# Kernel optimization log

Measured on AMD Instinct MI355X. Metric: run time of the kernel, lower is better.

Reference implementation:

```python
import jax, jax.numpy as jnp
import numpy as np

B, T, C = 2, 1024, 768
H, NE, K = 3072, 8, 2


def setup_inputs() -> dict:
    key = jax.random.key(0)
    k1, k2, k3, k4 = jax.random.split(key, 4)
    x = jax.random.normal(k1, (B, T, C), dtype=jnp.float32)
    w_fc = jax.random.normal(k2, (C, H * NE), dtype=jnp.float32) * 0.02
    w_proj = jax.random.normal(k3, (H * NE, C), dtype=jnp.float32) * (0.02 * (2 * 12) ** -0.5)
    w_gate = jax.random.normal(k4, (C, NE), dtype=jnp.float32) * 0.02
    return {"x": x, "w_fc": w_fc, "w_proj": w_proj, "w_gate": w_gate}


def reference(x, w_fc, w_proj, w_gate):
    # Router: softmax over experts, top-k, renormalize selected probs.
    router_logits = jnp.einsum('btc,ce->bte', x, w_gate)
    router_probs = jax.nn.softmax(router_logits, axis=-1)
    top_p, top_i = jax.lax.top_k(router_probs, K)          # (B,T,K)
    top_p = top_p / jnp.sum(top_p, axis=-1, keepdims=True)

    # First projection. Original gathers (C,H,B,T,K) weight slices then
    # einsum('btc,chbtk->bthk'); mathematically identical to projecting with
    # all experts and gathering the selected outputs (same contraction order).
    wf = w_fc.reshape(C, H, NE)
    h_all = jnp.einsum('btc,che->bthe', x, wf)             # (B,T,H,NE)
    h = jnp.take_along_axis(h_all, top_i[:, :, None, :], axis=-1)  # (B,T,H,K)
    h = jax.nn.gelu(h, approximate=True)

    # Second projection + weighted combine over the K selected experts.
    wp = w_proj.reshape(H, C, NE)
    o_all = jnp.einsum('bthk,hce->btcke', h, wp)           # (B,T,C,K,NE)
    o = jnp.take_along_axis(o_all, top_i[:, :, None, :, None], axis=-1)[..., 0]  # (B,T,C,K)
    o = jnp.einsum('btck,btk->btc', o, top_p)
    return o
```

## Files before the change

kernel.cpp:

```cpp
#include <hip/hip_runtime.h>
#include <hip/hip_bf16.h>
#include <math.h>

#define BB 2
#define TT 1024
#define CC 768
#define HH 3072
#define NEXP 8
#define NTOK (BB*TT)
#define CAP 1024
#define CNT_STRIDE 32

typedef __attribute__((ext_vector_type(8))) short short8;
typedef __attribute__((ext_vector_type(4))) float float4v;

typedef const __attribute__((address_space(1))) void* gptr_t;
typedef __attribute__((address_space(3))) void* sptr_t;

__device__ __forceinline__ unsigned short f2bf(float f) {
    unsigned int u = __float_as_uint(f);
    unsigned int r = (u + 0x7fffu + ((u >> 16) & 1u)) >> 16;
    return (unsigned short)r;
}
__device__ __forceinline__ float gelu_tanh(float v) {
    const float k2 = 2.0f * 0.7978845608028654f;
    const float k1 = 0.044715f;
    float z = k2 * (v + k1 * v * v * v);
    return v / (1.0f + __expf(-z));
}

__device__ __forceinline__ void permute_body(
        const float* __restrict__ In, unsigned short* __restrict__ Out,
        int Adim, int Bdim, int a0, int b0, unsigned short* L) {
    int t = threadIdx.x;
#pragma unroll
    for (int j = 0; j < 8; ++j) {
        int idx = j * 256 + t;
        int r = idx >> 4, c4 = idx & 15;
        const float4 v = *(const float4*)(In + (size_t)(a0 + r) * Bdim * 8 + b0 * 8 + c4 * 4);
        ushort2 s01, s23;
        s01.x = f2bf(v.x); s01.y = f2bf(v.y);
        s23.x = f2bf(v.z); s23.y = f2bf(v.w);
        *(ushort2*)&L[r * 66 + c4 * 4]     = s01;
        *(ushort2*)&L[r * 66 + c4 * 4 + 2] = s23;
    }
    __syncthreads();
    int w = t >> 6, ln = t & 63;
    int oc = w * 16 + (ln & 15);
    int e = oc & 7, b = b0 + (oc >> 3);
    unsigned short* dst = Out + ((size_t)e * Bdim + b) * Adim + a0;
#pragma unroll
    for (int p = 0; p < 4; ++p) {
        int seg = (ln >> 4) + p * 4;
        short8 vv;
#pragma unroll
        for (int k = 0; k < 8; ++k) vv[k] = (short)L[(seg * 8 + k) * 66 + oc];
        *(short8*)(dst + seg * 8) = vv;
    }
}

__device__ __forceinline__ void router_body(
        const float* __restrict__ x, const float* __restrict__ w_gate,
        float* __restrict__ top_p, int* __restrict__ counts,
        int* __restrict__ tok_list, int t) {
    int lane = threadIdx.x & 63;
    float acc[NEXP];
#pragma unroll
    for (int e = 0; e < NEXP; ++e) acc[e] = 0.f;
    for (int c = lane; c < CC; c += 64) {
        float xv = x[t * CC + c];
        const float4* wg = (const float4*)(w_gate + c * NEXP);
        float4 w0 = wg[0], w1 = wg[1];
        acc[0] += xv * w0.x; acc[1] += xv * w0.y;
        acc[2] += xv * w0.z; acc[3] += xv * w0.w;
        acc[4] += xv * w1.x; acc[5] += xv * w1.y;
        acc[6] += xv * w1.z; acc[7] += xv * w1.w;
    }
#pragma unroll
    for (int e = 0; e < NEXP; ++e) {
        for (int off = 32; off > 0; off >>= 1)
            acc[e] += __shfl_down(acc[e], off, 64);
    }
    if (lane == 0) {
        float m = acc[0];
#pragma unroll
        for (int e = 1; e < NEXP; ++e) m = fmaxf(m, acc[e]);
        float p[NEXP]; float s = 0.f;
#pragma unroll
        for (int e = 0; e < NEXP; ++e) { p[e] = expf(acc[e] - m); s += p[e]; }
        float inv_s = 1.f / s;
#pragma unroll
        for (int e = 0; e < NEXP; ++e) p[e] *= inv_s;
        int i0 = 0;
#pragma unroll
        for (int e = 1; e < NEXP; ++e) if (p[e] > p[i0]) i0 = e;
        int i1 = (i0 == 0) ? 1 : 0;
#pragma unroll
        for (int e = 0; e < NEXP; ++e) if (e != i0 && p[e] > p[i1]) i1 = e;
        float p0 = p[i0], p1 = p[i1];
        float inv = 1.f / (p0 + p1);
        top_p[t * 2 + 0] = p0 * inv;
        top_p[t * 2 + 1] = p1 * inv;
        int pos0 = atomicAdd(&counts[i0 * CNT_STRIDE], 1);
        if (pos0 < CAP) tok_list[i0 * NTOK + pos0] = t * 2 + 0;
        int pos1 = atomicAdd(&counts[i1 * CNT_STRIDE], 1);
        if (pos1 < CAP) tok_list[i1 * NTOK + pos1] = t * 2 + 1;
    }
}

__global__ __launch_bounds__(256)
void mega_pre(const float* __restrict__ w_fc, unsigned short* __restrict__ wfc_b,
              const float* __restrict__ w_proj, unsigned short* __restrict__ wp_b,
              const float* __restrict__ x, const float* __restrict__ w_gate,
              float* __restrict__ top_p, int* __restrict__ counts,
              int* __restrict__ tok_list) {
    __shared__ unsigned short L[128 * 66];
    int bid = blockIdx.x;
    if (bid < 2304) {
        permute_body(w_fc, wfc_b, CC, HH, (bid % 6) * 128, (bid / 6) * 8, L);
    } else if (bid < 4608) {
        int b2 = bid - 2304;
        permute_body(w_proj, wp_b, HH, CC, (b2 % 24) * 128, (b2 / 24) * 8, L);
    } else {
        int wave = threadIdx.x >> 6;
        int t = (bid - 4608) * 4 + wave;
        router_body(x, w_gate, top_p, counts, tok_list, t);
    }
}

__global__ void gather_x(const float* __restrict__ x,
                         const int* __restrict__ counts,
                         const int* __restrict__ tok_list,
                         unsigned short* __restrict__ xg) {
    int pos = blockIdx.x;
    int e = pos >> 10, i = pos & (CAP - 1);
    int M = counts[e * CNT_STRIDE]; if (M > CAP) M = CAP;
    int Mr = (M + 127) & ~127; if (Mr > CAP) Mr = CAP;
    if (i >= Mr) return;
    int c = threadIdx.x * 4;
    unsigned short* dst = xg + (size_t)pos * CC + c;
    ushort4 s;
    if (i < M) {
        int tk = tok_list[e * NTOK + i] >> 1;
        float4 v = *(const float4*)(x + (size_t)tk * CC + c);
        s.x = f2bf(v.x); s.y = f2bf(v.y); s.z = f2bf(v.z); s.w = f2bf(v.w);
    } else {
        s.x = s.y = s.z = s.w = 0;
    }
    *(ushort4*)dst = s;
}

__global__ __launch_bounds__(256)
void gemm1_mfma(const unsigned short* __restrict__ xg,
                const unsigned short* __restrict__ wfc_b,
                const int* __restrict__ counts,
                unsigned short* __restrict__ h_slab) {
    int e = blockIdx.z;
    int M = counts[e * CNT_STRIDE]; if (M > CAP) M = CAP;
    int m0 = blockIdx.y * 128;
    if (m0 >= M) return;
    int n0 = blockIdx.x * 128;

    __shared__ unsigned short As[2][128 * 32];
    __shared__ unsigned short Bs[2][128 * 32];

    int tid = threadIdx.x;
    int wave = tid >> 6, lane = tid & 63;
    int wm = wave >> 1, wn = wave & 1;
    int quad = lane >> 4, l16 = lane & 15;

    const unsigned short* aBase = xg + ((size_t)e * CAP + m0) * CC;
    const unsigned short* bBase = wfc_b + ((size_t)e * HH + n0) * CC;

    int srow = wave * 32 + (lane >> 2);
    int schunk = (lane & 3) * 8;

    float4v acc[4][4];
#pragma unroll
    for (int i = 0; i < 4; ++i)
#pragma unroll
        for (int j = 0; j < 4; ++j)
#pragma unroll
            for (int r = 0; r < 4; ++r) acc[i][j][r] = 0.f;

#pragma unroll
    for (int q = 0; q < 2; ++q) {
        int r = srow + q * 16;
        __builtin_amdgcn_global_load_lds(
            (gptr_t)(aBase + (size_t)r * CC + schunk),
            (sptr_t)(&As[0][(wave * 32 + q * 16) * 32]), 16, 0, 0);
        __builtin_amdgcn_global_load_lds(
            (gptr_t)(bBase + (size_t)r * CC + schunk),
            (sptr_t)(&Bs[0][(wave * 32 + q * 16) * 32]), 16, 0, 0);
    }

    for (int k0 = 0; k0 < CC; k0 += 32) {
        int cur = (k0 >> 5) & 1;
        __syncthreads();
        if (k0 + 32 < CC) {
            int nxt = cur ^ 1;
#pragma unroll
            for (int q = 0; q < 2; ++q) {
                int r = srow + q * 16;
                __builtin_amdgcn_global_load_lds(
                    (gptr_t)(aBase + (size_t)r * CC + k0 + 32 + schunk),
                    (sptr_t)(&As[nxt][(wave * 32 + q * 16) * 32]), 16, 0, 0);
                __builtin_amdgcn_global_load_lds(
                    (gptr_t)(bBase + (size_t)r * CC + k0 + 32 + schunk),
                    (sptr_t)(&Bs[nxt][(wave * 32 + q * 16) * 32]), 16, 0, 0);
            }
        }
        short8 af[4], bf[4];
#pragma unroll
        for (int mt = 0; mt < 4; ++mt)
            af[mt] = *(const short8*)&As[cur][(wm * 64 + mt * 16 + l16) * 32 + quad * 8];
#pragma unroll
        for (int nt = 0; nt < 4; ++nt)
            bf[nt] = *(const short8*)&Bs[cur][(wn * 64 + nt * 16 + l16) * 32 + quad * 8];
#pragma unroll
        for (int mt = 0; mt < 4; ++mt)
#pragma unroll
            for (int nt = 0; nt < 4; ++nt)
                acc[mt][nt] = __builtin_amdgcn_mfma_f32_16x16x32_bf16(
                    af[mt], bf[nt], acc[mt][nt], 0, 0, 0);
    }

#pragma unroll
    for (int mt = 0; mt < 4; ++mt) {
#pragma unroll
        for (int r = 0; r < 4; ++r) {
            int m = m0 + wm * 64 + mt * 16 + quad * 4 + r;
            unsigned short* orow = h_slab + ((size_t)e * CAP + m) * HH + n0 + wn * 64 + l16;
#pragma unroll
            for (int nt = 0; nt < 4; ++nt)
                orow[nt * 16] = f2bf(gelu_tanh(acc[mt][nt][r]));
        }
    }
}

__global__ __launch_bounds__(256)
void gemm2_mfma(const unsigned short* __restrict__ h_slab,
                const unsigned short* __restrict__ wp_b,
                const int* __restrict__ counts,
                const int* __restrict__ tok_list,
                float* __restrict__ o_part) {
    int e = blockIdx.z;
    int M = counts[e * CNT_STRIDE]; if (M > CAP) M = CAP;
    int m0 = blockIdx.y * 128;
    if (m0 >= M) return;
    int n0 = (blockIdx.x >> 2) * 128;
    int ks = blockIdx.x & 3;

    __shared__ unsigned short As[2][128 * 32];
    __shared__ unsigned short Bs[2][128 * 32];

    int tid = threadIdx.x;
    int wave = tid >> 6, lane = tid & 63;
    int wm = wave >> 1, wn = wave & 1;
    int quad = lane >> 4, l16 = lane & 15;

    const unsigned short* aBase = h_slab + ((size_t)e * CAP + m0) * HH + ks * 768;
    const unsigned short* bBase = wp_b + ((size_t)e * CC + n0) * HH + ks * 768;

    int srow = wave * 32 + (lane >> 2);
    int schunk = (lane & 3) * 8;

    float4v acc[4][4];
#pragma unroll
    for (int i = 0; i < 4; ++i)
#pragma unroll
        for (int j = 0; j < 4; ++j)
#pragma unroll
            for (int r = 0; r < 4; ++r) acc[i][j][r] = 0.f;

#pragma unroll
    for (int q = 0; q < 2; ++q) {
        int r = srow + q * 16;
        __builtin_amdgcn_global_load_lds(
            (gptr_t)(aBase + (size_t)r * HH + schunk),
            (sptr_t)(&As[0][(wave * 32 + q * 16) * 32]), 16, 0, 0);
        __builtin_amdgcn_global_load_lds(
            (gptr_t)(bBase + (size_t)r * HH + schunk),
            (sptr_t)(&Bs[0][(wave * 32 + q * 16) * 32]), 16, 0, 0);
    }

    for (int k0 = 0; k0 < 768; k0 += 32) {
        int cur = (k0 >> 5) & 1;
        __syncthreads();
        if (k0 + 32 < 768) {
            int nxt = cur ^ 1;
#pragma unroll
            for (int q = 0; q < 2; ++q) {
                int r = srow + q * 16;
                __builtin_amdgcn_global_load_lds(
                    (gptr_t)(aBase + (size_t)r * HH + k0 + 32 + schunk),
                    (sptr_t)(&As[nxt][(wave * 32 + q * 16) * 32]), 16, 0, 0);
                __builtin_amdgcn_global_load_lds(
                    (gptr_t)(bBase + (size_t)r * HH + k0 + 32 + schunk),
                    (sptr_t)(&Bs[nxt][(wave * 32 + q * 16) * 32]), 16, 0, 0);
            }
        }
        short8 af[4], bf[4];
#pragma unroll
        for (int mt = 0; mt < 4; ++mt)
            af[mt] = *(const short8*)&As[cur][(wm * 64 + mt * 16 + l16) * 32 + quad * 8];
#pragma unroll
        for (int nt = 0; nt < 4; ++nt)
            bf[nt] = *(const short8*)&Bs[cur][(wn * 64 + nt * 16 + l16) * 32 + quad * 8];
#pragma unroll
        for (int mt = 0; mt < 4; ++mt)
#pragma unroll
            for (int nt = 0; nt < 4; ++nt)
                acc[mt][nt] = __builtin_amdgcn_mfma_f32_16x16x32_bf16(
                    af[mt], bf[nt], acc[mt][nt], 0, 0, 0);
    }

#pragma unroll
    for (int mt = 0; mt < 4; ++mt) {
#pragma unroll
        for (int r = 0; r < 4; ++r) {
            int m = m0 + wm * 64 + mt * 16 + quad * 4 + r;
            if (m < M) {
                int ent = tok_list[e * NTOK + m];
                float* orow = o_part + ((size_t)ks * NTOK * 2 + ent) * CC + n0 + wn * 64 + l16;
#pragma unroll
                for (int nt = 0; nt < 4; ++nt)
                    orow[nt * 16] = acc[mt][nt][r];
            }
        }
    }
}

__global__ void combine_kernel(const float* __restrict__ o_part,
                               const float* __restrict__ top_p,
                               float* __restrict__ out) {
    int idx = blockIdx.x * 256 + threadIdx.x;
    int t = idx / (CC / 4);
    int c = (idx % (CC / 4)) * 4;
    float p0 = top_p[2 * t], p1 = top_p[2 * t + 1];
    float4 s0 = make_float4(0.f, 0.f, 0.f, 0.f);
    float4 s1 = make_float4(0.f, 0.f, 0.f, 0.f);
#pragma unroll
    for (int ks = 0; ks < 4; ++ks) {
        const float4 a = *(const float4*)(o_part + ((size_t)ks * NTOK * 2 + 2 * t) * CC + c);
        const float4 b = *(const float4*)(o_part + ((size_t)ks * NTOK * 2 + 2 * t + 1) * CC + c);
        s0.x += a.x; s0.y += a.y; s0.z += a.z; s0.w += a.w;
        s1.x += b.x; s1.y += b.y; s1.z += b.z; s1.w += b.w;
    }
    float4 r;
    r.x = p0 * s0.x + p1 * s1.x;
    r.y = p0 * s0.y + p1 * s1.y;
    r.z = p0 * s0.z + p1 * s1.z;
    r.w = p0 * s0.w + p1 * s1.w;
    *(float4*)(out + (size_t)t * CC + c) = r;
}

extern "C" void kernel_launch(void* const* d_in, const int* in_sizes, int n_in,
                              void* d_out, int out_size, void* d_ws, size_t ws_size,
                              hipStream_t stream) {
    const float* x      = (const float*)d_in[0];
    const float* w_fc   = (const float*)d_in[1];
    const float* w_proj = (const float*)d_in[2];
    const float* w_gate = (const float*)d_in[3];
    float* out = (float*)d_out;

    char* ws = (char*)d_ws;
    size_t off = 0;
    float* top_p    = (float*)(ws + off); off += NTOK * 2 * sizeof(float);
    int*   counts   = (int*)(ws + off);   off += CNT_STRIDE * NEXP * 4;
    int*   tok_list = (int*)(ws + off);   off += (size_t)NEXP * NTOK * 4;
    off = 131072;
    unsigned short* wp_b   = (unsigned short*)(ws + off); off += (size_t)NEXP*CC*HH*2;
    unsigned short* h_slab = (unsigned short*)(ws + off); off += (size_t)NEXP*CAP*HH*2;
    unsigned short* wfc_b  = (unsigned short*)(ws + off);
    float*          o_part = (float*)(ws + off);          off += (size_t)NEXP*HH*CC*2;
    unsigned short* xg     = (unsigned short*)(ws + off); off += (size_t)NEXP*CAP*CC*2;

    hipMemsetAsync(counts, 0, CNT_STRIDE * NEXP * 4, stream);

    mega_pre<<<2304 + 2304 + 512, 256, 0, stream>>>(
        w_fc, wfc_b, w_proj, wp_b, x, w_gate, top_p, counts, tok_list);

    gather_x<<<NEXP * CAP, 192, 0, stream>>>(x, counts, tok_list, xg);

    gemm1_mfma<<<dim3(HH / 128, CAP / 128, NEXP), 256, 0, stream>>>(
        xg, wfc_b, counts, h_slab);
    gemm2_mfma<<<dim3((CC / 128) * 4, CAP / 128, NEXP), 256, 0, stream>>>(
        h_slab, wp_b, counts, tok_list, o_part);
    combine_kernel<<<(NTOK * CC / 4) / 256, 256, 0, stream>>>(o_part, top_p, out);
}
```

Measured before the change: 287.7 us.

## Fold token gather into GEMM1 via per-row indirect loads from bf16 x

Drops the separate gather_x kernel, which wrote a padded per-expert bf16 copy of x. The pre-kernel now converts x to bf16 once per token and writes a zero row, and GEMM1 resolves each A-tile row's source pointer through tok_list, loading straight from the converted x or from the zero row for padding. This removes one launch and the gathered-buffer round trip through memory, at the cost of scattered row addresses in GEMM1's A loads and a workspace layout that now overlaps xb with the o_part region.

```diff
diff --git a/kernel.cpp b/kernel.cpp
--- a/kernel.cpp
+++ b/kernel.cpp
@@ -113,7 +113,8 @@
               const float* __restrict__ w_proj, unsigned short* __restrict__ wp_b,
               const float* __restrict__ x, const float* __restrict__ w_gate,
               float* __restrict__ top_p, int* __restrict__ counts,
-              int* __restrict__ tok_list) {
+              int* __restrict__ tok_list, unsigned short* __restrict__ xb,
+              unsigned short* __restrict__ zrow) {
     __shared__ unsigned short L[128 * 66];
     int bid = blockIdx.x;
     if (bid < 2304) {
@@ -121,39 +122,34 @@
     } else if (bid < 4608) {
         int b2 = bid - 2304;
         permute_body(w_proj, wp_b, HH, CC, (b2 % 24) * 128, (b2 / 24) * 8, L);
+    } else if (bid < 5120) {
+        int t = (bid - 4608) * 4 + (threadIdx.x >> 6);
+        router_body(x, w_gate, top_p, counts, tok_list, t);
+    } else if (bid < 5632) {
+        int t = (bid - 5120) * 4 + (threadIdx.x >> 6);
+        int lane = threadIdx.x & 63;
+#pragma unroll
+        for (int rnd = 0; rnd < 3; ++rnd) {
+            int c = rnd * 256 + lane * 4;
+            float4 v = *(const float4*)(x + (size_t)t * CC + c);
+            ushort4 s;
+            s.x = f2bf(v.x); s.y = f2bf(v.y); s.z = f2bf(v.z); s.w = f2bf(v.w);
+            *(ushort4*)(xb + (size_t)t * CC + c) = s;
+        }
     } else {
-        int wave = threadIdx.x >> 6;
-        int t = (bid - 4608) * 4 + wave;
-        router_body(x, w_gate, top_p, counts, tok_list, t);
-    }
-}
-
-__global__ void gather_x(const float* __restrict__ x,
-                         const int* __restrict__ counts,
-                         const int* __restrict__ tok_list,
-                         unsigned short* __restrict__ xg) {
-    int pos = blockIdx.x;
-    int e = pos >> 10, i = pos & (CAP - 1);
-    int M = counts[e * CNT_STRIDE]; if (M > CAP) M = CAP;
-    int Mr = (M + 127) & ~127; if (Mr > CAP) Mr = CAP;
-    if (i >= Mr) return;
-    int c = threadIdx.x * 4;
-    unsigned short* dst = xg + (size_t)pos * CC + c;
-    ushort4 s;
-    if (i < M) {
-        int tk = tok_list[e * NTOK + i] >> 1;
-        float4 v = *(const float4*)(x + (size_t)tk * CC + c);
-        s.x = f2bf(v.x); s.y = f2bf(v.y); s.z = f2bf(v.z); s.w = f2bf(v.w);
-    } else {
-        s.x = s.y = s.z = s.w = 0;
-    }
-    *(ushort4*)dst = s;
+        if (threadIdx.x < 192) {
+            ushort4 z; z.x = z.y = z.z = z.w = 0;
+            ((ushort4*)zrow)[threadIdx.x] = z;
+        }
+    }
 }
 
 __global__ __launch_bounds__(256)
-void gemm1_mfma(const unsigned short* __restrict__ xg,
+void gemm1_mfma(const unsigned short* __restrict__ xb,
                 const unsigned short* __restrict__ wfc_b,
                 const int* __restrict__ counts,
+                const int* __restrict__ tok_list,
+                const unsigned short* __restrict__ zrow,
                 unsigned short* __restrict__ h_slab) {
     int e = blockIdx.z;
     int M = counts[e * CNT_STRIDE]; if (M > CAP) M = CAP;
@@ -169,11 +165,22 @@
     int wm = wave >> 1, wn = wave & 1;
     int quad = lane >> 4, l16 = lane & 15;
 
-    const unsigned short* aBase = xg + ((size_t)e * CAP + m0) * CC;
     const unsigned short* bBase = wfc_b + ((size_t)e * HH + n0) * CC;
 
     int srow = wave * 32 + (lane >> 2);
     int schunk = (lane & 3) * 8;
+
+    const unsigned short* aSrc[2];
+#pragma unroll
+    for (int q = 0; q < 2; ++q) {
+        int m = m0 + srow + q * 16;
+        if (m < M) {
+            int tk = tok_list[e * NTOK + m] >> 1;
+            aSrc[q] = xb + (size_t)tk * CC + schunk;
+        } else {
+            aSrc[q] = zrow + schunk;
+        }
+    }
 
     float4v acc[4][4];
 #pragma unroll
@@ -187,7 +194,7 @@
     for (int q = 0; q < 2; ++q) {
         int r = srow + q * 16;
         __builtin_amdgcn_global_load_lds(
-            (gptr_t)(aBase + (size_t)r * CC + schunk),
+            (gptr_t)(aSrc[q]),
             (sptr_t)(&As[0][(wave * 32 + q * 16) * 32]), 16, 0, 0);
         __builtin_amdgcn_global_load_lds(
             (gptr_t)(bBase + (size_t)r * CC + schunk),
@@ -203,7 +210,7 @@
             for (int q = 0; q < 2; ++q) {
                 int r = srow + q * 16;
                 __builtin_amdgcn_global_load_lds(
-                    (gptr_t)(aBase + (size_t)r * CC + k0 + 32 + schunk),
+                    (gptr_t)(aSrc[q] + k0 + 32),
                     (sptr_t)(&As[nxt][(wave * 32 + q * 16) * 32]), 16, 0, 0);
                 __builtin_amdgcn_global_load_lds(
                     (gptr_t)(bBase + (size_t)r * CC + k0 + 32 + schunk),
@@ -369,22 +376,29 @@
     float* top_p    = (float*)(ws + off); off += NTOK * 2 * sizeof(float);
     int*   counts   = (int*)(ws + off);   off += CNT_STRIDE * NEXP * 4;
     int*   tok_list = (int*)(ws + off);   off += (size_t)NEXP * NTOK * 4;
+    unsigned short* zrow = (unsigned short*)(ws + 90112);
+
+    const size_t sz_wp  = (size_t)NEXP * CC * HH * 2;
+    const size_t sz_h   = (size_t)NEXP * CAP * HH * 2;
+    const size_t sz_wfc = (size_t)NEXP * HH * CC * 2;
+    const size_t sz_op  = (size_t)4 * NTOK * 2 * CC * 4;
+
     off = 131072;
-    unsigned short* wp_b   = (unsigned short*)(ws + off); off += (size_t)NEXP*CC*HH*2;
-    unsigned short* h_slab = (unsigned short*)(ws + off); off += (size_t)NEXP*CAP*HH*2;
+    unsigned short* wp_b   = (unsigned short*)(ws + off); off += sz_wp;
+    unsigned short* h_slab = (unsigned short*)(ws + off); off += sz_h;
     unsigned short* wfc_b  = (unsigned short*)(ws + off);
-    float*          o_part = (float*)(ws + off);          off += (size_t)NEXP*HH*CC*2;
-    unsigned short* xg     = (unsigned short*)(ws + off); off += (size_t)NEXP*CAP*CC*2;
+    float*          o_part = (float*)(ws + off);
+    unsigned short* xb     = (unsigned short*)(ws + off + sz_wfc);
+    off += sz_op;
 
     hipMemsetAsync(counts, 0, CNT_STRIDE * NEXP * 4, stream);
 
-    mega_pre<<<2304 + 2304 + 512, 256, 0, stream>>>(
-        w_fc, wfc_b, w_proj, wp_b, x, w_gate, top_p, counts, tok_list);
-
-    gather_x<<<NEXP * CAP, 192, 0, stream>>>(x, counts, tok_list, xg);
+    mega_pre<<<2304 + 2304 + 512 + 512 + 1, 256, 0, stream>>>(
+        w_fc, wfc_b, w_proj, wp_b, x, w_gate, top_p, counts, tok_list,
+        xb, zrow);
 
     gemm1_mfma<<<dim3(HH / 128, CAP / 128, NEXP), 256, 0, stream>>>(
-        xg, wfc_b, counts, h_slab);
+        xb, wfc_b, counts, tok_list, zrow, h_slab);
     gemm2_mfma<<<dim3((CC / 128) * 4, CAP / 128, NEXP), 256, 0, stream>>>(
         h_slab, wp_b, counts, tok_list, o_part);
     combine_kernel<<<(NTOK * CC / 4) / 256, 256, 0, stream>>>(o_part, top_p, out);
```

Measured after the change: 281.6 us. 2.1% less time.
